# Performance work log

Hardware: AMD Instinct MI355X
Metric: run time of the kernel (lower is better)

The kernel has to match this reference:

```python
import jax, jax.numpy as jnp
import numpy as np

P, B, I, O = 32, 512, 1024, 1024


def setup_inputs() -> dict:
    key = jax.random.key(0)
    kx, kw = jax.random.split(key)
    # strictly {0,1}-valued binary tensors stored as float32, as in the torch module
    x = (jax.random.uniform(kx, (P, B, I)) > 0.5).astype(jnp.float32)
    w = (jax.random.uniform(kw, (2, P, I, O)) > 0.5).astype(jnp.float32)
    return {"x": x, "w": w}


def reference(x, w):
    # x: [P, B, I] binary; w: [2, P, I, O] binary.
    # out = x @ W0 + (~x) @ W1  (logical_not of a {0,1} float is 1 - x)
    notx = 1.0 - x
    out = jnp.einsum('pbi,pio->pbo', x, w[0]) + jnp.einsum('pbi,pio->pbo', notx, w[1])
    return out  # [P, B, O], activation == 'none'
```

## Files before the change

kernel.cpp:

```cpp
#include <hip/hip_runtime.h>


namespace {

constexpr int PP = 32;
constexpr int BB = 512;
constexpr int II = 1024;
constexpr int OO = 1024;

constexpr int BM = 256;
constexpr int BN = 256;
constexpr int BK = 32;

constexpr int KPA = 40;

__device__ __forceinline__ int boff(int o, int k) {
    return o * 40 + (o >> 2) * 8 + k;
}

typedef __attribute__((ext_vector_type(8))) short bf16x8;
typedef __attribute__((ext_vector_type(4))) float f32x4;

constexpr int A_BYTES = BM * KPA * 2;
constexpr int B_BYTES = (BN * 40 + (BN / 4) * 8) * 2;
constexpr int SMEM_BYTES = A_BYTES + B_BYTES;

__device__ __forceinline__ unsigned pk2(float lo, float hi) {
    return (__float_as_uint(lo) >> 16) | (__float_as_uint(hi) & 0xFFFF0000u);
}

__global__ __launch_bounds__(1024) void ebl_kernel(const float* __restrict__ x,
                                                   const float* __restrict__ w,
                                                   float* __restrict__ out) {
    __shared__ __align__(16) char smem[SMEM_BYTES];
    unsigned short* As = (unsigned short*)smem;
    unsigned short* Bs = (unsigned short*)(smem + A_BYTES);
    float* Scr    = (float*)smem;
    float* ColSum = (float*)(smem + 16384);

    const int t  = (int)threadIdx.x;
    const int l  = t & 63;
    const int wv = t >> 6;
    const int wm = wv & 3;
    const int wn = wv >> 2;
    const int lq = l >> 4;
    const int ln = l & 15;

    const int bid = (int)blockIdx.x;
    const int wid = (bid & 7) * 32 + (bid >> 3);
    const int p   = wid >> 3;
    const int o0  = ((wid >> 1) & 3) * BN;
    const int b0  = (wid & 1) * BM;

    const float* xp  = x + ((size_t)p * BB + b0) * II;
    const float* w0p = w + (size_t)p * II * OO;
    const float* w1p = w + (size_t)(PP + p) * II * OO;

    const int a_row = t >> 3;
    const int a_col = (t & 7) * 4;
    const int b_colg = 4 * l;

    int a_rd[4], b_rd[4];
#pragma unroll
    for (int mt = 0; mt < 4; ++mt)
        a_rd[mt] = (wm * 64 + mt * 16 + ln) * KPA + lq * 8;
#pragma unroll
    for (int nt = 0; nt < 4; ++nt)
        b_rd[nt] = boff(wn * 64 + nt * 16 + ln, lq * 8);

    f32x4 acc[4][4];
#pragma unroll
    for (int mt = 0; mt < 4; ++mt)
#pragma unroll
        for (int nt = 0; nt < 4; ++nt)
            acc[mt][nt] = (f32x4){0.f, 0.f, 0.f, 0.f};

    f32x4 csum = (f32x4){0.f, 0.f, 0.f, 0.f};

    const float* xa0  = xp + (size_t)a_row * II + a_col;
    const float* xa1  = xp + (size_t)(a_row + 128) * II + a_col;
    const float* wb00 = w0p + (size_t)(2 * wv) * OO + o0 + b_colg;
    const float* wb01 = w0p + (size_t)(2 * wv + 1) * OO + o0 + b_colg;
    const float* wb10 = w1p + (size_t)(2 * wv) * OO + o0 + b_colg;
    const float* wb11 = w1p + (size_t)(2 * wv + 1) * OO + o0 + b_colg;

    for (int kk = 0; kk < II; kk += BK) {
        f32x4 a0  = *(const f32x4*)(xa0 + kk);
        f32x4 a1  = *(const f32x4*)(xa1 + kk);
        f32x4 p00 = *(const f32x4*)(wb00 + (size_t)kk * OO);
        f32x4 p01 = *(const f32x4*)(wb01 + (size_t)kk * OO);
        f32x4 p10 = *(const f32x4*)(wb10 + (size_t)kk * OO);
        f32x4 p11 = *(const f32x4*)(wb11 + (size_t)kk * OO);

        __syncthreads();

        *(uint2*)(&As[a_row * KPA + a_col]) =
            make_uint2(pk2(a0.x, a0.y), pk2(a0.z, a0.w));
        *(uint2*)(&As[(a_row + 128) * KPA + a_col]) =
            make_uint2(pk2(a1.x, a1.y), pk2(a1.z, a1.w));

        f32x4 d0 = p00 - p10;
        f32x4 d1 = p01 - p11;
        csum += p10;
        csum += p11;
        const int kloc = 2 * wv;
#pragma unroll
        for (int c = 0; c < 4; ++c)
            *(unsigned*)(&Bs[boff(b_colg + c, kloc)]) = pk2(d0[c], d1[c]);

        __syncthreads();

        bf16x8 af[4], bfm[4];
#pragma unroll
        for (int mt = 0; mt < 4; ++mt)
            af[mt] = *(const bf16x8*)(&As[a_rd[mt]]);
#pragma unroll
        for (int nt = 0; nt < 4; ++nt)
            bfm[nt] = *(const bf16x8*)(&Bs[b_rd[nt]]);
#pragma unroll
        for (int mt = 0; mt < 4; ++mt)
#pragma unroll
            for (int nt = 0; nt < 4; ++nt)
                acc[mt][nt] = __builtin_amdgcn_mfma_f32_16x16x32_bf16(
                    af[mt], bfm[nt], acc[mt][nt], 0, 0, 0);
    }

    __syncthreads();
    *(f32x4*)(&Scr[wv * 256 + l * 4]) = csum;
    __syncthreads();
    if (t < 256) {
        float s = 0.f;
#pragma unroll
        for (int ww = 0; ww < 16; ++ww) s += Scr[ww * 256 + t];
        ColSum[t] = s;
    }
    __syncthreads();

    float* op = out + (size_t)p * BB * OO + o0;
#pragma unroll
    for (int nt = 0; nt < 4; ++nt) {
        const int ocol = wn * 64 + nt * 16 + ln;
        const float cs = ColSum[ocol];
#pragma unroll
        for (int mt = 0; mt < 4; ++mt) {
            const int row = b0 + wm * 64 + mt * 16 + lq * 4;
#pragma unroll
            for (int r = 0; r < 4; ++r)
                op[(size_t)(row + r) * OO + ocol] = acc[mt][nt][r] + cs;
        }
    }
}

}

extern "C" void kernel_launch(void* const* d_in, const int* in_sizes, int n_in,
                              void* d_out, int out_size, void* d_ws, size_t ws_size,
                              hipStream_t stream) {
    const float* x = (const float*)d_in[0];
    const float* w = (const float*)d_in[1];
    float* out = (float*)d_out;
    dim3 grid(PP * (BB / BM) * (OO / BN), 1, 1);
    ebl_kernel<<<grid, dim3(1024, 1, 1), 0, stream>>>(x, w, out);
}
```

Baseline: 430.8 us.

## Reshape block tile to full batch rows so each weight column is read once

Changes the block tile from 256x256 to 512x128, so each block covers the whole batch dimension and every weight element is fetched by exactly one block instead of two. Weight loads become 2-wide nontemporal loads, and x rows are loaded four per thread. The intent is to halve global weight traffic, since the weights dominate the input bytes. In exchange each block rereads x more often across the O dimension, there is less B-fragment reuse per wave (8x2 MFMA tiles), and the grid stays at 256 blocks.

```diff
diff --git a/kernel.cpp b/kernel.cpp
--- a/kernel.cpp
+++ b/kernel.cpp
@@ -8,8 +8,8 @@
 constexpr int II = 1024;
 constexpr int OO = 1024;
 
-constexpr int BM = 256;
-constexpr int BN = 256;
+constexpr int BM = 512;
+constexpr int BN = 128;
 constexpr int BK = 32;
 
 constexpr int KPA = 40;
@@ -20,6 +20,7 @@
 
 typedef __attribute__((ext_vector_type(8))) short bf16x8;
 typedef __attribute__((ext_vector_type(4))) float f32x4;
+typedef __attribute__((ext_vector_type(2))) float f32x2;
 
 constexpr int A_BYTES = BM * KPA * 2;
 constexpr int B_BYTES = (BN * 40 + (BN / 4) * 8) * 2;
@@ -36,7 +37,7 @@
     unsigned short* As = (unsigned short*)smem;
     unsigned short* Bs = (unsigned short*)(smem + A_BYTES);
     float* Scr    = (float*)smem;
-    float* ColSum = (float*)(smem + 16384);
+    float* ColSum = (float*)(smem + 8192);
 
     const int t  = (int)threadIdx.x;
     const int l  = t & 63;
@@ -49,48 +50,51 @@
     const int bid = (int)blockIdx.x;
     const int wid = (bid & 7) * 32 + (bid >> 3);
     const int p   = wid >> 3;
-    const int o0  = ((wid >> 1) & 3) * BN;
-    const int b0  = (wid & 1) * BM;
+    const int o0  = (wid & 7) * BN;
 
-    const float* xp  = x + ((size_t)p * BB + b0) * II;
+    const float* xp  = x + (size_t)p * BB * II;
     const float* w0p = w + (size_t)p * II * OO;
     const float* w1p = w + (size_t)(PP + p) * II * OO;
 
     const int a_row = t >> 3;
     const int a_col = (t & 7) * 4;
-    const int b_colg = 4 * l;
+    const int oc = 2 * l;
 
-    int a_rd[4], b_rd[4];
+    int a_rd[8], b_rd[2];
 #pragma unroll
-    for (int mt = 0; mt < 4; ++mt)
-        a_rd[mt] = (wm * 64 + mt * 16 + ln) * KPA + lq * 8;
+    for (int mt = 0; mt < 8; ++mt)
+        a_rd[mt] = (wm * 128 + mt * 16 + ln) * KPA + lq * 8;
 #pragma unroll
-    for (int nt = 0; nt < 4; ++nt)
-        b_rd[nt] = boff(wn * 64 + nt * 16 + ln, lq * 8);
+    for (int nt = 0; nt < 2; ++nt)
+        b_rd[nt] = boff(wn * 32 + nt * 16 + ln, lq * 8);
 
-    f32x4 acc[4][4];
+    f32x4 acc[8][2];
 #pragma unroll
-    for (int mt = 0; mt < 4; ++mt)
+    for (int mt = 0; mt < 8; ++mt)
 #pragma unroll
-        for (int nt = 0; nt < 4; ++nt)
+        for (int nt = 0; nt < 2; ++nt)
             acc[mt][nt] = (f32x4){0.f, 0.f, 0.f, 0.f};
 
-    f32x4 csum = (f32x4){0.f, 0.f, 0.f, 0.f};
+    f32x2 csum = (f32x2){0.f, 0.f};
 
     const float* xa0  = xp + (size_t)a_row * II + a_col;
-    const float* xa1  = xp + (size_t)(a_row + 128) * II + a_col;
-    const float* wb00 = w0p + (size_t)(2 * wv) * OO + o0 + b_colg;
-    const float* wb01 = w0p + (size_t)(2 * wv + 1) * OO + o0 + b_colg;
-    const float* wb10 = w1p + (size_t)(2 * wv) * OO + o0 + b_colg;
-    const float* wb11 = w1p + (size_t)(2 * wv + 1) * OO + o0 + b_colg;
+    const float* xa1  = xa0 + (size_t)128 * II;
+    const float* xa2  = xa0 + (size_t)256 * II;
+    const float* xa3  = xa0 + (size_t)384 * II;
+    const float* wb00 = w0p + (size_t)(2 * wv) * OO + o0 + oc;
+    const float* wb01 = w0p + (size_t)(2 * wv + 1) * OO + o0 + oc;
+    const float* wb10 = w1p + (size_t)(2 * wv) * OO + o0 + oc;
+    const float* wb11 = w1p + (size_t)(2 * wv + 1) * OO + o0 + oc;
 
     for (int kk = 0; kk < II; kk += BK) {
-        f32x4 a0  = *(const f32x4*)(xa0 + kk);
-        f32x4 a1  = *(const f32x4*)(xa1 + kk);
-        f32x4 p00 = *(const f32x4*)(wb00 + (size_t)kk * OO);
-        f32x4 p01 = *(const f32x4*)(wb01 + (size_t)kk * OO);
-        f32x4 p10 = *(const f32x4*)(wb10 + (size_t)kk * OO);
-        f32x4 p11 = *(const f32x4*)(wb11 + (size_t)kk * OO);
+        f32x4 a0 = *(const f32x4*)(xa0 + kk);
+        f32x4 a1 = *(const f32x4*)(xa1 + kk);
+        f32x4 a2 = *(const f32x4*)(xa2 + kk);
+        f32x4 a3 = *(const f32x4*)(xa3 + kk);
+        f32x2 q00 = __builtin_nontemporal_load((const f32x2*)(wb00 + (size_t)kk * OO));
+        f32x2 q01 = __builtin_nontemporal_load((const f32x2*)(wb01 + (size_t)kk * OO));
+        f32x2 q10 = __builtin_nontemporal_load((const f32x2*)(wb10 + (size_t)kk * OO));
+        f32x2 q11 = __builtin_nontemporal_load((const f32x2*)(wb11 + (size_t)kk * OO));
 
         __syncthreads();
 
@@ -98,52 +102,55 @@
             make_uint2(pk2(a0.x, a0.y), pk2(a0.z, a0.w));
         *(uint2*)(&As[(a_row + 128) * KPA + a_col]) =
             make_uint2(pk2(a1.x, a1.y), pk2(a1.z, a1.w));
+        *(uint2*)(&As[(a_row + 256) * KPA + a_col]) =
+            make_uint2(pk2(a2.x, a2.y), pk2(a2.z, a2.w));
+        *(uint2*)(&As[(a_row + 384) * KPA + a_col]) =
+            make_uint2(pk2(a3.x, a3.y), pk2(a3.z, a3.w));
 
-        f32x4 d0 = p00 - p10;
-        f32x4 d1 = p01 - p11;
-        csum += p10;
-        csum += p11;
+        f32x2 d0 = q00 - q10;
+        f32x2 d1 = q01 - q11;
+        csum += q10;
+        csum += q11;
         const int kloc = 2 * wv;
 #pragma unroll
-        for (int c = 0; c < 4; ++c)
-            *(unsigned*)(&Bs[boff(b_colg + c, kloc)]) = pk2(d0[c], d1[c]);
+        for (int c = 0; c < 2; ++c)
+            *(unsigned*)(&Bs[boff(oc + c, kloc)]) = pk2(d0[c], d1[c]);
 
         __syncthreads();
 
-        bf16x8 af[4], bfm[4];
+        bf16x8 bfm[2];
 #pragma unroll
-        for (int mt = 0; mt < 4; ++mt)
-            af[mt] = *(const bf16x8*)(&As[a_rd[mt]]);
-#pragma unroll
-        for (int nt = 0; nt < 4; ++nt)
+        for (int nt = 0; nt < 2; ++nt)
             bfm[nt] = *(const bf16x8*)(&Bs[b_rd[nt]]);
 #pragma unroll
-        for (int mt = 0; mt < 4; ++mt)
+        for (int mt = 0; mt < 8; ++mt) {
+            bf16x8 af = *(const bf16x8*)(&As[a_rd[mt]]);
 #pragma unroll
-            for (int nt = 0; nt < 4; ++nt)
+            for (int nt = 0; nt < 2; ++nt)
                 acc[mt][nt] = __builtin_amdgcn_mfma_f32_16x16x32_bf16(
-                    af[mt], bfm[nt], acc[mt][nt], 0, 0, 0);
+                    af, bfm[nt], acc[mt][nt], 0, 0, 0);
+        }
     }
 
     __syncthreads();
-    *(f32x4*)(&Scr[wv * 256 + l * 4]) = csum;
+    *(f32x2*)(&Scr[wv * 128 + oc]) = csum;
     __syncthreads();
-    if (t < 256) {
+    if (t < 128) {
         float s = 0.f;
 #pragma unroll
-        for (int ww = 0; ww < 16; ++ww) s += Scr[ww * 256 + t];
+        for (int q = 0; q < 16; ++q) s += Scr[q * 128 + t];
         ColSum[t] = s;
     }
     __syncthreads();
 
     float* op = out + (size_t)p * BB * OO + o0;
 #pragma unroll
-    for (int nt = 0; nt < 4; ++nt) {
-        const int ocol = wn * 64 + nt * 16 + ln;
+    for (int nt = 0; nt < 2; ++nt) {
+        const int ocol = wn * 32 + nt * 16 + ln;
         const float cs = ColSum[ocol];
 #pragma unroll
-        for (int mt = 0; mt < 4; ++mt) {
-            const int row = b0 + wm * 64 + mt * 16 + lq * 4;
+        for (int mt = 0; mt < 8; ++mt) {
+            const int row = wm * 128 + mt * 16 + lq * 4;
 #pragma unroll
             for (int r = 0; r < 4; ++r)
                 op[(size_t)(row + r) * OO + ocol] = acc[mt][nt][r] + cs;
@@ -159,6 +166,6 @@
     const float* x = (const float*)d_in[0];
     const float* w = (const float*)d_in[1];
     float* out = (float*)d_out;
-    dim3 grid(PP * (BB / BM) * (OO / BN), 1, 1);
+    dim3 grid(PP * (OO / BN), 1, 1);
     ebl_kernel<<<grid, dim3(1024, 1, 1), 0, stream>>>(x, w, out);
 }
```

New measurement: 440.7 us. 2.3% more time.
